# Optimization experiments

Measured on AMD Instinct MI355X. Metric: run time of the kernel, lower is better.

The kernel has to match this reference:

```python
import jax, jax.numpy as jnp
import numpy as np

NUM_OPS, B, T, D = 8, 8, 512, 1024


def setup_inputs() -> dict:
    key = jax.random.key(0)
    k1, k2, k3, k4 = jax.random.split(key, 4)
    x = jax.random.normal(k1, (B, T, D), dtype=jnp.float32)
    W = jax.random.normal(k2, (NUM_OPS, D, D), dtype=jnp.float32) * 0.02
    b = jnp.zeros((NUM_OPS, D), dtype=jnp.float32)
    logits = 0.001 * jax.random.normal(k3, (NUM_OPS,), dtype=jnp.float32)
    # uniform noise for Gumbel sampling (matches tf.random.uniform in sample_without_replacement)
    u = jax.random.uniform(k4, (NUM_OPS,), dtype=jnp.float32, minval=1e-6, maxval=1.0 - 1e-6)
    return {"x": x, "W": W, "b": b, "logits": logits, "u": u}


def reference(x, W, b, logits, u):
    # weights = softmax(logits); gumbel top-1 over log(weights) == log_softmax(logits)
    gumbel = -jnp.log(-jnp.log(u))
    idx = jnp.argmax(jax.nn.log_softmax(logits) + gumbel)
    # forward of ops_times_mask_binary: sum over ON ops (num_on_samples=1 -> single op)
    out = jnp.einsum('btd,de->bte', x, W[idx]) + b[idx]  # [B,T,D]
    return out
```

## Files before the change

kernel.cpp:

```cpp
#include <hip/hip_runtime.h>

typedef unsigned short u16;
typedef unsigned int u32;
typedef __attribute__((ext_vector_type(8))) short bf16x8;
typedef __attribute__((ext_vector_type(4))) float f32x4;

#define NUM_OPS 8
#define M_DIM 4096
#define K_DIM 1024
#define N_DIM 1024
#define BK 32
#define KITERS (K_DIM / BK)


__device__ __forceinline__ u16 f2b(float f) {
  union { float f; u32 u; } v; v.f = f;
  u32 r = v.u + 0x7fffu + ((v.u >> 16) & 1u);
  return (u16)(r >> 16);
}

__device__ __forceinline__ u32 pk2(float a, float b) {
  return (u32)f2b(a) | ((u32)f2b(b) << 16);
}

__device__ __forceinline__ int compute_idx(const float* __restrict__ logits,
                                           const float* __restrict__ u) {
  int best = 0; float bv = -3.4e38f;
#pragma unroll
  for (int i = 0; i < NUM_OPS; ++i) {
    float v = logits[i] - logf(-logf(u[i]));
    if (v > bv) { bv = v; best = i; }
  }
  return best;
}

__device__ __forceinline__ void gld_lds16(const void* g, void* l) {
  __builtin_amdgcn_global_load_lds(
      (__attribute__((address_space(1))) void*)(g),
      (__attribute__((address_space(3))) void*)(unsigned)(unsigned long long)(l),
      16, 0, 0);
}

__global__ void prep_kernel(const float* __restrict__ x, const float* __restrict__ W,
                            const float* __restrict__ logits, const float* __restrict__ u,
                            u16* __restrict__ xb, u16* __restrict__ wt) {
  const int tid = threadIdx.x;
  const int bid = blockIdx.x;
  if (bid < 2048) {
    const int chunk = bid * 4 + (tid >> 6), l = tid & 63;
    const int mtile = chunk >> 5, ktile = chunk & 31;
    const float* src = x + (size_t)(mtile * 16 + (l & 15)) * K_DIM
                         + ktile * 32 + (l >> 4) * 8;
    float4 f0 = *(const float4*)(src);
    float4 f1 = *(const float4*)(src + 4);
    uint4 p;
    p.x = pk2(f0.x, f0.y); p.y = pk2(f0.z, f0.w);
    p.z = pk2(f1.x, f1.y); p.w = pk2(f1.z, f1.w);
    *(uint4*)(xb + (size_t)chunk * 512 + l * 8) = p;
  } else {
    __shared__ u16 t[64][66];
    const int wb = bid - 2048;
    const int kt = wb >> 4, nt = wb & 15;
    const int idx = compute_idx(logits, u);
    const float* Wi = W + (size_t)idx * K_DIM * N_DIM;
#pragma unroll
    for (int it = 0; it < 16; ++it) {
      int i = it * 256 + tid;
      int r = i >> 6, c = i & 63;
      t[r][c] = f2b(Wi[(size_t)(kt * 64 + r) * N_DIM + nt * 64 + c]);
    }
    __syncthreads();
#pragma unroll
    for (int it = 0; it < 2; ++it) {
      int s = it * 256 + tid;
      int c = s >> 6, l = s & 63;
      int ntl = c & 3, ktl = c >> 2;
      int kb = ktl * 32 + (l >> 4) * 8, nn = ntl * 16 + (l & 15);
      uint4 p;
      p.x = (u32)t[kb + 0][nn] | ((u32)t[kb + 1][nn] << 16);
      p.y = (u32)t[kb + 2][nn] | ((u32)t[kb + 3][nn] << 16);
      p.z = (u32)t[kb + 4][nn] | ((u32)t[kb + 5][nn] << 16);
      p.w = (u32)t[kb + 6][nn] | ((u32)t[kb + 7][nn] << 16);
      int chunk = (nt * 4 + ntl) * 32 + (kt * 2 + ktl);
      *(uint4*)(wt + (size_t)chunk * 512 + l * 8) = p;
    }
  }
}

__global__ __launch_bounds__(256) void gemm_kernel(
    const u16* __restrict__ xb, const u16* __restrict__ wt,
    const float* __restrict__ bvec, const float* __restrict__ logits,
    const float* __restrict__ u, float* __restrict__ out) {
  __shared__ u16 sB[2][4 * 512];

  const int tid = threadIdx.x;
  const int w = tid >> 6, L = tid & 63;
  const int bid = blockIdx.x;
  const int mb = (bid & 7) * 4 + ((bid >> 3) & 3);
  const int nb = bid >> 5;
  const int m0 = mb * 128, n0 = nb * 64;

  const u16* gA0 = xb + ((size_t)(mb * 8 + 2 * w) * 32) * 512 + L * 8;
  const u16* gA1 = gA0 + 32 * 512;
  const u16* gB = wt + ((size_t)(nb * 4 + w) * 32) * 512 + L * 8;
  const int lB = w * 512 + L * 8;

  f32x4 acc[2][4] = {};

  gld_lds16(gB, &sB[0][lB]);
  bf16x8 ra[2][2];
  ra[0][0] = *(const bf16x8*)(gA0);
  ra[0][1] = *(const bf16x8*)(gA1);

  for (int kk = 0; kk < KITERS; ++kk) {
    const int cur = kk & 1, nxt = cur ^ 1;
    __syncthreads();

    if (kk + 1 < KITERS) {
      const int ko = (kk + 1) * 512;
      gld_lds16(gB + ko, &sB[nxt][lB]);
      ra[nxt][0] = *(const bf16x8*)(gA0 + ko);
      ra[nxt][1] = *(const bf16x8*)(gA1 + ko);
    }

    bf16x8 bf[4];
#pragma unroll
    for (int t = 0; t < 4; ++t) bf[t] = *(const bf16x8*)(&sB[cur][t * 512 + L * 8]);
#pragma unroll
    for (int f = 0; f < 2; ++f)
#pragma unroll
      for (int t = 0; t < 4; ++t)
        acc[f][t] = __builtin_amdgcn_mfma_f32_16x16x32_bf16(
            ra[cur][f], bf[t], acc[f][t], 0, 0, 0);
  }

  const int idx = compute_idx(logits, u);
  const float* bi = bvec + (size_t)idx * N_DIM;
#pragma unroll
  for (int f = 0; f < 2; ++f) {
    int row = m0 + 32 * w + 16 * f + (L >> 4) * 4;
#pragma unroll
    for (int t = 0; t < 4; ++t) {
      int col = n0 + 16 * t + (L & 15);
      float bv = bi[col];
#pragma unroll
      for (int r = 0; r < 4; ++r)
        out[(size_t)(row + r) * N_DIM + col] = acc[f][t][r] + bv;
    }
  }
}


extern "C" void kernel_launch(void* const* d_in, const int* in_sizes, int n_in,
                              void* d_out, int out_size, void* d_ws, size_t ws_size,
                              hipStream_t stream) {
  const float* x      = (const float*)d_in[0];
  const float* W      = (const float*)d_in[1];
  const float* bvec   = (const float*)d_in[2];
  const float* logits = (const float*)d_in[3];
  const float* u      = (const float*)d_in[4];
  float* out = (float*)d_out;

  u16* xb = (u16*)d_ws;
  u16* wt = (u16*)d_ws + (size_t)M_DIM * K_DIM;

  prep_kernel<<<2048 + 256, 256, 0, stream>>>(x, W, logits, u, xb, wt);
  gemm_kernel<<<512, 256, 0, stream>>>(xb, wt, bvec, logits, u, out);
}
```

Before: 109.5 us.

## Replace LDS-staged GEMM with per-wave 64x64 register tiles loaded directly from global

The GEMM drops shared-memory staging and block-wide barriers. Each wave now computes a 64x64 output tile with a 4x4 MFMA fragment grid, loading A and B fragments straight from global memory into double-buffered registers. The grid halves to 256 blocks, and the block-to-tile mapping is rearranged so that a block's four waves share the same M rows. The aim is to remove barrier and LDS overhead and raise MFMA work per fragment load. The costs are higher register pressure, 256 blocks (about one per CU), and each wave re-reading A from global/L2 with no LDS sharing.

```diff
diff --git a/kernel.cpp b/kernel.cpp
--- a/kernel.cpp
+++ b/kernel.cpp
@@ -9,8 +9,7 @@
 #define M_DIM 4096
 #define K_DIM 1024
 #define N_DIM 1024
-#define BK 32
-#define KITERS (K_DIM / BK)
+#define KT 32
 
 
 __device__ __forceinline__ u16 f2b(float f) {
@@ -32,13 +31,6 @@
     if (v > bv) { bv = v; best = i; }
   }
   return best;
-}
-
-__device__ __forceinline__ void gld_lds16(const void* g, void* l) {
-  __builtin_amdgcn_global_load_lds(
-      (__attribute__((address_space(1))) void*)(g),
-      (__attribute__((address_space(3))) void*)(unsigned)(unsigned long long)(l),
-      16, 0, 0);
 }
 
 __global__ void prep_kernel(const float* __restrict__ x, const float* __restrict__ W,
@@ -91,61 +83,61 @@
     const u16* __restrict__ xb, const u16* __restrict__ wt,
     const float* __restrict__ bvec, const float* __restrict__ logits,
     const float* __restrict__ u, float* __restrict__ out) {
-  __shared__ u16 sB[2][4 * 512];
-
   const int tid = threadIdx.x;
   const int w = tid >> 6, L = tid & 63;
   const int bid = blockIdx.x;
-  const int mb = (bid & 7) * 4 + ((bid >> 3) & 3);
-  const int nb = bid >> 5;
-  const int m0 = mb * 128, n0 = nb * 64;
+  const int x7 = bid & 7, r = bid >> 3;
+  const int mt = x7 * 8 + (r >> 2);
+  const int nt = (r & 3) * 4 + w;
 
-  const u16* gA0 = xb + ((size_t)(mb * 8 + 2 * w) * 32) * 512 + L * 8;
-  const u16* gA1 = gA0 + 32 * 512;
-  const u16* gB = wt + ((size_t)(nb * 4 + w) * 32) * 512 + L * 8;
-  const int lB = w * 512 + L * 8;
+  const u16* pa[4];
+  const u16* pb[4];
+#pragma unroll
+  for (int f = 0; f < 4; ++f) {
+    pa[f] = xb + ((size_t)(mt * 4 + f) * 32) * 512 + L * 8;
+    pb[f] = wt + ((size_t)(nt * 4 + f) * 32) * 512 + L * 8;
+  }
 
-  f32x4 acc[2][4] = {};
+  f32x4 acc[4][4] = {};
+  bf16x8 af[2][4], bf[2][4];
 
-  gld_lds16(gB, &sB[0][lB]);
-  bf16x8 ra[2][2];
-  ra[0][0] = *(const bf16x8*)(gA0);
-  ra[0][1] = *(const bf16x8*)(gA1);
+#pragma unroll
+  for (int f = 0; f < 4; ++f) {
+    af[0][f] = *(const bf16x8*)(pa[f]);
+    bf[0][f] = *(const bf16x8*)(pb[f]);
+  }
 
-  for (int kk = 0; kk < KITERS; ++kk) {
-    const int cur = kk & 1, nxt = cur ^ 1;
-    __syncthreads();
-
-    if (kk + 1 < KITERS) {
-      const int ko = (kk + 1) * 512;
-      gld_lds16(gB + ko, &sB[nxt][lB]);
-      ra[nxt][0] = *(const bf16x8*)(gA0 + ko);
-      ra[nxt][1] = *(const bf16x8*)(gA1 + ko);
+#pragma unroll
+  for (int kt = 0; kt < KT; ++kt) {
+    const int cur = kt & 1, nxt = cur ^ 1;
+    if (kt + 1 < KT) {
+      const int ko = (kt + 1) * 512;
+#pragma unroll
+      for (int f = 0; f < 4; ++f) {
+        af[nxt][f] = *(const bf16x8*)(pa[f] + ko);
+        bf[nxt][f] = *(const bf16x8*)(pb[f] + ko);
+      }
     }
-
-    bf16x8 bf[4];
 #pragma unroll
-    for (int t = 0; t < 4; ++t) bf[t] = *(const bf16x8*)(&sB[cur][t * 512 + L * 8]);
+    for (int mf = 0; mf < 4; ++mf)
 #pragma unroll
-    for (int f = 0; f < 2; ++f)
-#pragma unroll
-      for (int t = 0; t < 4; ++t)
-        acc[f][t] = __builtin_amdgcn_mfma_f32_16x16x32_bf16(
-            ra[cur][f], bf[t], acc[f][t], 0, 0, 0);
+      for (int nf = 0; nf < 4; ++nf)
+        acc[mf][nf] = __builtin_amdgcn_mfma_f32_16x16x32_bf16(
+            af[cur][mf], bf[cur][nf], acc[mf][nf], 0, 0, 0);
   }
 
   const int idx = compute_idx(logits, u);
   const float* bi = bvec + (size_t)idx * N_DIM;
 #pragma unroll
-  for (int f = 0; f < 2; ++f) {
-    int row = m0 + 32 * w + 16 * f + (L >> 4) * 4;
+  for (int mf = 0; mf < 4; ++mf) {
+    int row = mt * 64 + 16 * mf + (L >> 4) * 4;
 #pragma unroll
-    for (int t = 0; t < 4; ++t) {
-      int col = n0 + 16 * t + (L & 15);
+    for (int nf = 0; nf < 4; ++nf) {
+      int col = nt * 64 + 16 * nf + (L & 15);
       float bv = bi[col];
 #pragma unroll
-      for (int r = 0; r < 4; ++r)
-        out[(size_t)(row + r) * N_DIM + col] = acc[f][t][r] + bv;
+      for (int rr = 0; rr < 4; ++rr)
+        out[(size_t)(row + rr) * N_DIM + col] = acc[mf][nf][rr] + bv;
     }
   }
 }
@@ -165,5 +157,5 @@
   u16* wt = (u16*)d_ws + (size_t)M_DIM * K_DIM;
 
   prep_kernel<<<2048 + 256, 256, 0, stream>>>(x, W, logits, u, xb, wt);
-  gemm_kernel<<<512, 256, 0, stream>>>(xb, wt, bvec, logits, u, out);
+  gemm_kernel<<<256, 256, 0, stream>>>(xb, wt, bvec, logits, u, out);
 }
```

After: 122.7 us. +12.0%, slower.
